# Optimization experiments

Hardware: AMD Instinct MI355X
Metric: run time of the kernel (lower is better)

Reference implementation:

```python
import jax, jax.numpy as jnp
import numpy as np

NUM_EXPERTS = 8
HIDDEN = 2048
INTER = 4096
TOKENS = 4096
TOP_K = 2


def setup_inputs() -> dict:
    key = jax.random.key(0)
    ks = jax.random.split(key, 6)
    x = jax.random.normal(ks[0], (TOKENS, HIDDEN), dtype=jnp.float32)
    expert_weights = jax.random.uniform(ks[1], (TOKENS, TOP_K), dtype=jnp.float32)
    expert_indices = jax.random.randint(ks[2], (TOKENS, TOP_K), 0, NUM_EXPERTS)
    # kaiming_uniform-ish init for stacked expert weights
    b1 = float(np.sqrt(6.0 / HIDDEN))
    b2 = float(np.sqrt(6.0 / INTER))
    w1_stacked = jax.random.uniform(ks[3], (NUM_EXPERTS, HIDDEN, INTER), minval=-b1, maxval=b1, dtype=jnp.float32)
    w2_stacked = jax.random.uniform(ks[4], (NUM_EXPERTS, INTER, HIDDEN), minval=-b2, maxval=b2, dtype=jnp.float32)
    w3_stacked = jax.random.uniform(ks[5], (NUM_EXPERTS, HIDDEN, INTER), minval=-b1, maxval=b1, dtype=jnp.float32)
    return {
        "x": x,
        "expert_weights": expert_weights,
        "w1_stacked": w1_stacked,
        "w2_stacked": w2_stacked,
        "w3_stacked": w3_stacked,
        "expert_indices": expert_indices,
        "num_experts_per_tok": TOP_K,
    }


def reference(x, expert_weights, w1_stacked, w2_stacked, w3_stacked, expert_indices, num_experts_per_tok):
    # out[t] = sum_k expert_weights[t,k] * SwiGLU_FFN_{expert_indices[t,k]}(x[t])
    # Loop over the small fixed expert set; masked weighted combine per expert.
    num_experts = w1_stacked.shape[0]
    out = jnp.zeros_like(x)
    for e in range(num_experts):
        gate = jax.nn.silu(x @ w1_stacked[e])          # [T, I]
        up = x @ w3_stacked[e]                          # [T, I]
        y = (gate * up) @ w2_stacked[e]                 # [T, H]
        # per-token routing weight for expert e (sum over top-k slots)
        w_e = jnp.sum(jnp.where(expert_indices == e, expert_weights, 0.0), axis=1)  # [T]
        out = out + w_e[:, None] * y
    return out
```

## Files before the change

### kernel.cpp

```cpp
#include <hip/hip_runtime.h>
#include <hip/hip_bf16.h>
#include <cstdint>

#define T_TOKENS 4096
#define HID      2048
#define INTER    4096
#define NEXP     8
#define TOPK     2
#define NPAIRS   (T_TOKENS * TOPK)
#define BM 256
#define BN 128
#define BK 64
#define MAXROWS  (NPAIRS + NEXP * BM)
#define NRB2     32

typedef __attribute__((ext_vector_type(8))) short   short8;
typedef __attribute__((ext_vector_type(4))) float   f32x4;
typedef __attribute__((ext_vector_type(8))) ushort  ushort8v;

static __device__ __forceinline__ ushort f2bf(float f) {
    __hip_bfloat16 b = __float2bfloat16(f);
    return __builtin_bit_cast(ushort, b);
}

typedef const __attribute__((address_space(1))) unsigned char ga_u8;
typedef __attribute__((address_space(3))) unsigned char       la_u8;
static __device__ __forceinline__ void gl_lds16(const void* g, void* l) {
    __builtin_amdgcn_global_load_lds((ga_u8*)g, (la_u8*)l, 16, 0, 0);
}

#define SBAR() do { __builtin_amdgcn_sched_barrier(0); \
                    __builtin_amdgcn_s_barrier(); \
                    __builtin_amdgcn_sched_barrier(0); \
                    asm volatile("" ::: "memory"); } while (0)
#define VMCNT(n) do { asm volatile("s_waitcnt vmcnt(" #n ")" ::: "memory"); \
                      __builtin_amdgcn_sched_barrier(0); } while (0)

__global__ void route_kernel(const int* __restrict__ eidx,
                             const float* __restrict__ ew,
                             int* __restrict__ cnt, int* __restrict__ pbase,
                             int* __restrict__ tokl, float* __restrict__ wgtl) {
    __shared__ int s_cnt[NEXP];
    __shared__ int s_pos[NEXP];
    __shared__ int s_base[NEXP];
    int tid = threadIdx.x;
    if (tid < NEXP) { s_cnt[tid] = 0; s_pos[tid] = 0; }
    __syncthreads();
    for (int p = tid; p < NPAIRS; p += blockDim.x)
        atomicAdd(&s_cnt[eidx[p]], 1);
    __syncthreads();
    if (tid == 0) {
        int b = 0;
        for (int e = 0; e < NEXP; ++e) {
            s_base[e] = b;
            cnt[e]    = s_cnt[e];
            pbase[e]  = b;
            b += (s_cnt[e] + BM - 1) / BM * BM;
        }
        pbase[NEXP] = b;
    }
    __syncthreads();
    for (int p = tid; p < NPAIRS; p += blockDim.x) {
        int e   = eidx[p];
        int pos = atomicAdd(&s_pos[e], 1);
        int row = s_base[e] + pos;
        tokl[row] = p >> 1;
        wgtl[row] = ew[p];
    }
}

__global__ __launch_bounds__(256) void cvt_x_kernel(const float* __restrict__ x,
                                                    ushort* __restrict__ xbf) {
    int i = (blockIdx.x * 256 + threadIdx.x) * 8;
    float4 a = *reinterpret_cast<const float4*>(x + i);
    float4 b = *reinterpret_cast<const float4*>(x + i + 4);
    ushort8v o;
    o[0] = f2bf(a.x); o[1] = f2bf(a.y); o[2] = f2bf(a.z); o[3] = f2bf(a.w);
    o[4] = f2bf(b.x); o[5] = f2bf(b.y); o[6] = f2bf(b.z); o[7] = f2bf(b.w);
    *reinterpret_cast<ushort8v*>(xbf + i) = o;
}

__global__ __launch_bounds__(256) void transpose_cvt_kernel(
        const float* __restrict__ src, ushort* __restrict__ dst,
        int K, int N, int c0, int CN, long estride) {
    int ez = blockIdx.z;
    const float* s = src + (size_t)ez * estride;
    ushort* d = dst + (size_t)ez * CN * K;
    int nb = blockIdx.x * 64 + c0;
    int kb = blockIdx.y * 64;
    __shared__ ushort t[64][72];
    int tid = threadIdx.x;
    int kr = tid >> 2;
    int ns = tid & 3;
    #pragma unroll
    for (int p = 0; p < 4; ++p) {
        int f = ns + p * 4;
        float4 v = *reinterpret_cast<const float4*>(&s[(size_t)(kb + kr) * N + nb + f * 4]);
        t[f * 4 + 0][kr] = f2bf(v.x);
        t[f * 4 + 1][kr] = f2bf(v.y);
        t[f * 4 + 2][kr] = f2bf(v.z);
        t[f * 4 + 3][kr] = f2bf(v.w);
    }
    __syncthreads();
    int nr = tid >> 2;
    #pragma unroll
    for (int p = 0; p < 2; ++p) {
        int ks = ((tid & 3) + p * 4) * 8;
        ushort8v v8 = *reinterpret_cast<const ushort8v*>(&t[nr][ks]);
        *reinterpret_cast<ushort8v*>(&d[(size_t)(nb - c0 + nr) * K + kb + ks]) = v8;
    }
}

__global__ __launch_bounds__(512, 2) void ffn1_kernel(
        const ushort* __restrict__ xbf,
        const ushort* __restrict__ wT1, const ushort* __restrict__ wT3,
        const int* __restrict__ cnt, const int* __restrict__ pbase,
        const int* __restrict__ tokl, ushort* __restrict__ h,
        int ncb, int c0) {
    int d = blockIdx.x;
    int xcd = d & 7, q = d >> 3;
    int gq = q / NRB2, rb = q % NRB2;
    int g = gq * 8 + xcd;
    int ez = g / ncb, cb = g - ez * ncb;
    int ce = cnt[ez];
    int e = ez;
    (void)e;
    int r0 = rb * BM;
    if (r0 >= ce) return;
    int base = pbase[ez];

    __shared__ char lds[131072];
    char* Lb = lds;

    int tid  = threadIdx.x;
    int lane = tid & 63, wid = tid >> 6;
    int wr = (wid >> 1) * 64, wc = (wid & 1) * 64;
    int rlow = lane & 15, khi = lane >> 4;

    int rr = tid >> 3;
    int ss = (tid & 7) ^ (rr & 7);
    const ushort* pA[4];
    #pragma unroll
    for (int i = 0; i < 4; ++i) {
        int row = r0 + i * 64 + rr;
        int tok = (row < ce) ? tokl[base + row] : 0;
        pA[i] = xbf + (size_t)tok * HID + ss * 8;
    }
    size_t wrow = (size_t)ez * ((size_t)ncb * 128) + (size_t)cb * 128;
    const ushort* pB1[2];
    const ushort* pB3[2];
    #pragma unroll
    for (int i = 0; i < 2; ++i) {
        pB1[i] = wT1 + (wrow + i * 64 + rr) * HID + ss * 8;
        pB3[i] = wT3 + (wrow + i * 64 + rr) * HID + ss * 8;
    }
    int ldst = wid << 10;

    int aoffs[4][2], boffs[4][2];
    #pragma unroll
    for (int mi = 0; mi < 4; ++mi)
        #pragma unroll
        for (int kh = 0; kh < 2; ++kh) {
            int sw = (((kh << 2) + khi) ^ (lane & 7)) << 4;
            aoffs[mi][kh] = (wr + mi * 16 + rlow) * 128 + sw;
            boffs[mi][kh] = (wc + mi * 16 + rlow) * 128 + sw;
        }

    f32x4 accg[4][4], accu[4][4];
    #pragma unroll
    for (int i = 0; i < 4; ++i)
        #pragma unroll
        for (int j = 0; j < 4; ++j) { accg[i][j] = (f32x4)0.f; accu[i][j] = (f32x4)0.f; }

    {
        char* L = Lb;
        #pragma unroll
        for (int i = 0; i < 4; ++i) gl_lds16(pA[i], L + i * 8192 + ldst);
        #pragma unroll
        for (int i = 0; i < 2; ++i) gl_lds16(pB1[i], L + 32768 + i * 8192 + ldst);
        #pragma unroll
        for (int i = 0; i < 2; ++i) gl_lds16(pB3[i], L + 49152 + i * 8192 + ldst);
    }

    const int NT = HID / BK;
    #pragma unroll 1
    for (int t = 0; t < NT; ++t) {
        char* Lc = Lb + ((t & 1) ? 65536 : 0);
        char* Ln = Lb + ((t & 1) ? 0 : 65536);
        int adv = (t + 1) * 64;
        bool more = (t + 1 < NT);
        if (more) {
            gl_lds16(pA[0] + adv, Ln + 0 * 8192 + ldst);
            gl_lds16(pA[1] + adv, Ln + 1 * 8192 + ldst);
            VMCNT(2);
        } else {
            VMCNT(0);
        }
        SBAR();
        short8 af[4][2];
        #pragma unroll
        for (int mi = 0; mi < 4; ++mi)
            #pragma unroll
            for (int kh = 0; kh < 2; ++kh)
                af[mi][kh] = *reinterpret_cast<const short8*>(Lc + aoffs[mi][kh]);
        short8 bf[2][2];
        #pragma unroll
        for (int ni = 0; ni < 2; ++ni)
            #pragma unroll
            for (int kh = 0; kh < 2; ++kh)
                bf[ni][kh] = *reinterpret_cast<const short8*>(Lc + 32768 + boffs[ni][kh]);
        if (more) {
            gl_lds16(pA[2] + adv, Ln + 2 * 8192 + ldst);
            gl_lds16(pA[3] + adv, Ln + 3 * 8192 + ldst);
        }
        __builtin_amdgcn_s_setprio(1);
        #pragma unroll
        for (int ni = 0; ni < 2; ++ni)
            #pragma unroll
            for (int mi = 0; mi < 4; ++mi)
                #pragma unroll
                for (int kh = 0; kh < 2; ++kh)
                    accg[mi][ni] = __builtin_amdgcn_mfma_f32_16x16x32_bf16(af[mi][kh], bf[ni][kh], accg[mi][ni], 0, 0, 0);
        __builtin_amdgcn_s_setprio(0);
        SBAR();
        #pragma unroll
        for (int ni = 0; ni < 2; ++ni)
            #pragma unroll
            for (int kh = 0; kh < 2; ++kh)
                bf[ni][kh] = *reinterpret_cast<const short8*>(Lc + 49152 + boffs[ni][kh]);
        if (more) {
            gl_lds16(pB1[0] + adv, Ln + 32768 + ldst);
            gl_lds16(pB1[1] + adv, Ln + 32768 + 8192 + ldst);
        }
        __builtin_amdgcn_s_setprio(1);
        #pragma unroll
        for (int ni = 0; ni < 2; ++ni)
            #pragma unroll
            for (int mi = 0; mi < 4; ++mi)
                #pragma unroll
                for (int kh = 0; kh < 2; ++kh)
                    accu[mi][ni] = __builtin_amdgcn_mfma_f32_16x16x32_bf16(af[mi][kh], bf[ni][kh], accu[mi][ni], 0, 0, 0);
        __builtin_amdgcn_s_setprio(0);
        SBAR();
        #pragma unroll
        for (int ni = 0; ni < 2; ++ni)
            #pragma unroll
            for (int kh = 0; kh < 2; ++kh)
                bf[ni][kh] = *reinterpret_cast<const short8*>(Lc + 32768 + boffs[ni + 2][kh]);
        if (more) {
            gl_lds16(pB3[0] + adv, Ln + 49152 + ldst);
            gl_lds16(pB3[1] + adv, Ln + 49152 + 8192 + ldst);
        }
        __builtin_amdgcn_s_setprio(1);
        #pragma unroll
        for (int ni = 0; ni < 2; ++ni)
            #pragma unroll
            for (int mi = 0; mi < 4; ++mi)
                #pragma unroll
                for (int kh = 0; kh < 2; ++kh)
                    accg[mi][ni + 2] = __builtin_amdgcn_mfma_f32_16x16x32_bf16(af[mi][kh], bf[ni][kh], accg[mi][ni + 2], 0, 0, 0);
        __builtin_amdgcn_s_setprio(0);
        SBAR();
        #pragma unroll
        for (int ni = 0; ni < 2; ++ni)
            #pragma unroll
            for (int kh = 0; kh < 2; ++kh)
                bf[ni][kh] = *reinterpret_cast<const short8*>(Lc + 49152 + boffs[ni + 2][kh]);
        __builtin_amdgcn_s_setprio(1);
        #pragma unroll
        for (int ni = 0; ni < 2; ++ni)
            #pragma unroll
            for (int mi = 0; mi < 4; ++mi)
                #pragma unroll
                for (int kh = 0; kh < 2; ++kh)
                    accu[mi][ni + 2] = __builtin_amdgcn_mfma_f32_16x16x32_bf16(af[mi][kh], bf[ni][kh], accu[mi][ni + 2], 0, 0, 0);
        __builtin_amdgcn_s_setprio(0);
        SBAR();
    }

    int hcol = c0 + cb * 128 + wc + rlow;
    #pragma unroll
    for (int mi = 0; mi < 4; ++mi) {
        #pragma unroll
        for (int q2 = 0; q2 < 4; ++q2) {
            int r = r0 + wr + mi * 16 + khi * 4 + q2;
            if (r >= ce) continue;
            ushort* hp = h + (size_t)(base + r) * INTER + hcol;
            #pragma unroll
            for (int ni = 0; ni < 4; ++ni) {
                float gg = accg[mi][ni][q2];
                float uu = accu[mi][ni][q2];
                float s = gg / (1.f + __expf(-gg));
                hp[ni * 16] = f2bf(s * uu);
            }
        }
    }
}

__global__ __launch_bounds__(512, 2) void ffn2_kernel(
        const ushort* __restrict__ h,
        const ushort* __restrict__ wT2,
        const int* __restrict__ cnt, const int* __restrict__ pbase,
        const int* __restrict__ tokl, const float* __restrict__ wgtl,
        float* __restrict__ out, int ncb, int c0) {
    int d = blockIdx.x;
    int xcd = d & 7, q = d >> 3;
    int gq = q / NRB2, rb = q % NRB2;
    int g = gq * 8 + xcd;
    int ez = g / ncb, cb = g - ez * ncb;
    int ce = cnt[ez];
    int r0 = rb * BM;
    if (r0 >= ce) return;
    int base = pbase[ez];

    __shared__ char lds[98304];
    char* Lb = lds;

    int tid  = threadIdx.x;
    int lane = tid & 63, wid = tid >> 6;
    int wr = (wid >> 1) * 64, wc = (wid & 1) * 64;
    int rlow = lane & 15, khi = lane >> 4;

    int rr = tid >> 3;
    int ss = (tid & 7) ^ (rr & 7);
    const ushort* pA[4];
    #pragma unroll
    for (int i = 0; i < 4; ++i)
        pA[i] = h + (size_t)(base + r0 + i * 64 + rr) * INTER + ss * 8;
    size_t wrow = (size_t)ez * ((size_t)ncb * 128) + (size_t)cb * 128;
    const ushort* pB[2];
    #pragma unroll
    for (int i = 0; i < 2; ++i)
        pB[i] = wT2 + (wrow + i * 64 + rr) * INTER + ss * 8;
    int ldst = wid << 10;

    int aoffs[4][2], boffs[4][2];
    #pragma unroll
    for (int mi = 0; mi < 4; ++mi)
        #pragma unroll
        for (int kh = 0; kh < 2; ++kh) {
            int sw = (((kh << 2) + khi) ^ (lane & 7)) << 4;
            aoffs[mi][kh] = (wr + mi * 16 + rlow) * 128 + sw;
            boffs[mi][kh] = (wc + mi * 16 + rlow) * 128 + sw;
        }

    f32x4 acc[4][4];
    #pragma unroll
    for (int i = 0; i < 4; ++i)
        #pragma unroll
        for (int j = 0; j < 4; ++j) acc[i][j] = (f32x4)0.f;

    {
        char* L = Lb;
        #pragma unroll
        for (int i = 0; i < 4; ++i) gl_lds16(pA[i], L + i * 8192 + ldst);
        #pragma unroll
        for (int i = 0; i < 2; ++i) gl_lds16(pB[i], L + 32768 + i * 8192 + ldst);
    }

    const int NT = INTER / BK;
    #pragma unroll 1
    for (int t = 0; t < NT; ++t) {
        char* Lc = Lb + ((t & 1) ? 49152 : 0);
        char* Ln = Lb + ((t & 1) ? 0 : 49152);
        int adv = (t + 1) * 64;
        bool more = (t + 1 < NT);
        if (more) {
            gl_lds16(pA[0] + adv, Ln + 0 * 8192 + ldst);
            gl_lds16(pA[1] + adv, Ln + 1 * 8192 + ldst);
            VMCNT(2);
        } else {
            VMCNT(0);
        }
        SBAR();
        short8 af[4][2];
        #pragma unroll
        for (int mi = 0; mi < 4; ++mi)
            #pragma unroll
            for (int kh = 0; kh < 2; ++kh)
                af[mi][kh] = *reinterpret_cast<const short8*>(Lc + aoffs[mi][kh]);
        short8 bf[2][2];
        #pragma unroll
        for (int ni = 0; ni < 2; ++ni)
            #pragma unroll
            for (int kh = 0; kh < 2; ++kh)
                bf[ni][kh] = *reinterpret_cast<const short8*>(Lc + 32768 + boffs[ni][kh]);
        if (more) {
            gl_lds16(pA[2] + adv, Ln + 2 * 8192 + ldst);
            gl_lds16(pA[3] + adv, Ln + 3 * 8192 + ldst);
        }
        __builtin_amdgcn_s_setprio(1);
        #pragma unroll
        for (int ni = 0; ni < 2; ++ni)
            #pragma unroll
            for (int mi = 0; mi < 4; ++mi)
                #pragma unroll
                for (int kh = 0; kh < 2; ++kh)
                    acc[mi][ni] = __builtin_amdgcn_mfma_f32_16x16x32_bf16(af[mi][kh], bf[ni][kh], acc[mi][ni], 0, 0, 0);
        __builtin_amdgcn_s_setprio(0);
        SBAR();
        #pragma unroll
        for (int ni = 0; ni < 2; ++ni)
            #pragma unroll
            for (int kh = 0; kh < 2; ++kh)
                bf[ni][kh] = *reinterpret_cast<const short8*>(Lc + 32768 + boffs[ni + 2][kh]);
        if (more) {
            gl_lds16(pB[0] + adv, Ln + 32768 + ldst);
            gl_lds16(pB[1] + adv, Ln + 32768 + 8192 + ldst);
        }
        __builtin_amdgcn_s_setprio(1);
        #pragma unroll
        for (int ni = 0; ni < 2; ++ni)
            #pragma unroll
            for (int mi = 0; mi < 4; ++mi)
                #pragma unroll
                for (int kh = 0; kh < 2; ++kh)
                    acc[mi][ni + 2] = __builtin_amdgcn_mfma_f32_16x16x32_bf16(af[mi][kh], bf[ni][kh], acc[mi][ni + 2], 0, 0, 0);
        __builtin_amdgcn_s_setprio(0);
        SBAR();
    }

    int ocol = c0 + cb * 128 + wc + rlow;
    #pragma unroll
    for (int mi = 0; mi < 4; ++mi) {
        #pragma unroll
        for (int q2 = 0; q2 < 4; ++q2) {
            int r = r0 + wr + mi * 16 + khi * 4 + q2;
            if (r >= ce) continue;
            int tok  = tokl[base + r];
            float wv = wgtl[base + r];
            float* op = out + (size_t)tok * HID + ocol;
            #pragma unroll
            for (int ni = 0; ni < 4; ++ni)
                atomicAdd(&op[ni * 16], wv * acc[mi][ni][q2]);
        }
    }
}

extern "C" void kernel_launch(void* const* d_in, const int* in_sizes, int n_in,
                              void* d_out, int out_size, void* d_ws, size_t ws_size,
                              hipStream_t stream) {
    (void)in_sizes; (void)n_in; (void)out_size;
    const float* x   = (const float*)d_in[0];
    const float* ew  = (const float*)d_in[1];
    const float* w1  = (const float*)d_in[2];
    const float* w2  = (const float*)d_in[3];
    const float* w3  = (const float*)d_in[4];
    const int*  eidx = (const int*)d_in[5];
    float* out = (float*)d_out;

    int*   cnt   = (int*)d_ws;
    int*   pbase = cnt + 8;
    int*   tokl  = cnt + 32;
    float* wgtl  = (float*)(tokl + MAXROWS);
    ushort* xbf  = (ushort*)((((uintptr_t)(wgtl + MAXROWS)) + 255) & ~(uintptr_t)255);
    ushort* h    = xbf + (size_t)T_TOKENS * HID;
    ushort* region = h + (size_t)MAXROWS * INTER;
    size_t region_bytes = ws_size - ((char*)region - (char*)d_ws);

    hipMemsetAsync(d_out, 0, (size_t)T_TOKENS * HID * sizeof(float), stream);
    route_kernel<<<1, 256, 0, stream>>>(eidx, ew, cnt, pbase, tokl, wgtl);
    cvt_x_kernel<<<T_TOKENS * HID / 8 / 256, 256, 0, stream>>>(x, xbf);

    const size_t per_e1 = (size_t)2 * INTER * HID * 2;
    const size_t per_e2 = (size_t)HID * INTER * 2;

    if (region_bytes >= per_e1) {
        int EG = (int)(region_bytes / per_e1); if (EG > 8) EG = 8;
        for (int g = 0; g < NEXP; g += EG) {
            int ne = (NEXP - g < EG) ? (NEXP - g) : EG;
            ushort* wt1 = region;
            ushort* wt3 = region + (size_t)ne * INTER * HID;
            transpose_cvt_kernel<<<dim3(INTER / 64, HID / 64, ne), 256, 0, stream>>>(
                w1 + (size_t)g * HID * INTER, wt1, HID, INTER, 0, INTER, (long)HID * INTER);
            transpose_cvt_kernel<<<dim3(INTER / 64, HID / 64, ne), 256, 0, stream>>>(
                w3 + (size_t)g * HID * INTER, wt3, HID, INTER, 0, INTER, (long)HID * INTER);
            ffn1_kernel<<<NRB2 * ne * (INTER / BN), 512, 0, stream>>>(
                xbf, wt1, wt3, cnt + g, pbase + g, tokl, h, INTER / BN, 0);
        }
    } else {
        const int CN = 1024;
        for (int e = 0; e < NEXP; ++e) {
            for (int c = 0; c < INTER; c += CN) {
                ushort* wt1 = region;
                ushort* wt3 = region + (size_t)CN * HID;
                transpose_cvt_kernel<<<dim3(CN / 64, HID / 64, 1), 256, 0, stream>>>(
                    w1 + (size_t)e * HID * INTER, wt1, HID, INTER, c, CN, (long)HID * INTER);
                transpose_cvt_kernel<<<dim3(CN / 64, HID / 64, 1), 256, 0, stream>>>(
                    w3 + (size_t)e * HID * INTER, wt3, HID, INTER, c, CN, (long)HID * INTER);
                ffn1_kernel<<<NRB2 * (CN / BN), 512, 0, stream>>>(
                    xbf, wt1, wt3, cnt + e, pbase + e, tokl, h, CN / BN, c);
            }
        }
    }

    if (region_bytes >= per_e2) {
        int EG = (int)(region_bytes / per_e2); if (EG > 8) EG = 8;
        for (int g = 0; g < NEXP; g += EG) {
            int ne = (NEXP - g < EG) ? (NEXP - g) : EG;
            ushort* wt2 = region;
            transpose_cvt_kernel<<<dim3(HID / 64, INTER / 64, ne), 256, 0, stream>>>(
                w2 + (size_t)g * INTER * HID, wt2, INTER, HID, 0, HID, (long)INTER * HID);
            ffn2_kernel<<<NRB2 * ne * (HID / BN), 512, 0, stream>>>(
                h, wt2, cnt + g, pbase + g, tokl, wgtl, out, HID / BN, 0);
        }
    } else {
        const int CN = 1024;
        for (int e = 0; e < NEXP; ++e) {
            for (int c = 0; c < HID; c += CN) {
                ushort* wt2 = region;
                transpose_cvt_kernel<<<dim3(CN / 64, INTER / 64, 1), 256, 0, stream>>>(
                    w2 + (size_t)e * INTER * HID, wt2, INTER, HID, c, CN, (long)INTER * HID);
                ffn2_kernel<<<NRB2 * (CN / BN), 512, 0, stream>>>(
                    h, wt2, cnt + e, pbase + e, tokl, wgtl, out, CN / BN, c);
            }
        }
    }
}
```

Baseline: 873.0 us.

## Unify FFN GEMMs into templated 256x256 tile kernel with split gate/up passes

Replaces the fused gate+up kernel and the separate down-projection kernel with one templated GEMM using 256x256 tiles, 8 waves arranged 2x4, and a reworked four-phase pipeline in which A and B loads are staggered two tiles ahead. The gate and up projections become two separate launches: the first writes the gate result to h in bf16, the second reads it back and applies SiLU times up. The larger tile is meant to raise MFMA work per LDS byte. In exchange x is loaded twice, h makes an extra bf16 round trip through memory, and the gate value is rounded to bf16 before SiLU.

```diff
diff --git a/kernel.cpp b/kernel.cpp
--- a/kernel.cpp
+++ b/kernel.cpp
@@ -8,10 +8,8 @@
 #define NEXP     8
 #define TOPK     2
 #define NPAIRS   (T_TOKENS * TOPK)
-#define BM 256
-#define BN 128
-#define BK 64
-#define MAXROWS  (NPAIRS + NEXP * BM)
+#define BMR      256
+#define MAXROWS  (NPAIRS + NEXP * BMR)
 #define NRB2     32
 
 typedef __attribute__((ext_vector_type(8))) short   short8;
@@ -21,6 +19,9 @@
 static __device__ __forceinline__ ushort f2bf(float f) {
     __hip_bfloat16 b = __float2bfloat16(f);
     return __builtin_bit_cast(ushort, b);
+}
+static __device__ __forceinline__ float bf2f(ushort u) {
+    return __builtin_bit_cast(float, ((uint)u) << 16);
 }
 
 typedef const __attribute__((address_space(1))) unsigned char ga_u8;
@@ -35,6 +36,8 @@
                     asm volatile("" ::: "memory"); } while (0)
 #define VMCNT(n) do { asm volatile("s_waitcnt vmcnt(" #n ")" ::: "memory"); \
                       __builtin_amdgcn_sched_barrier(0); } while (0)
+#define LGKM0() do { asm volatile("s_waitcnt lgkmcnt(0)" ::: "memory"); \
+                     __builtin_amdgcn_sched_barrier(0); } while (0)
 
 __global__ void route_kernel(const int* __restrict__ eidx,
                              const float* __restrict__ ew,
@@ -55,7 +58,7 @@
             s_base[e] = b;
             cnt[e]    = s_cnt[e];
             pbase[e]  = b;
-            b += (s_cnt[e] + BM - 1) / BM * BM;
+            b += (s_cnt[e] + BMR - 1) / BMR * BMR;
         }
         pbase[NEXP] = b;
     }
@@ -111,328 +114,187 @@
     }
 }
 
-__global__ __launch_bounds__(512, 2) void ffn1_kernel(
-        const ushort* __restrict__ xbf,
-        const ushort* __restrict__ wT1, const ushort* __restrict__ wT3,
+template<int MODE>
+__global__ __launch_bounds__(512, 2) void gemm_kernel(
+        const ushort* __restrict__ Asrc, const ushort* __restrict__ wT,
         const int* __restrict__ cnt, const int* __restrict__ pbase,
-        const int* __restrict__ tokl, ushort* __restrict__ h,
-        int ncb, int c0) {
+        const int* __restrict__ tokl, const float* __restrict__ wgtl,
+        ushort* __restrict__ hbuf, float* __restrict__ out,
+        int ncb, int c0, int ng) {
+    constexpr int K  = (MODE == 2) ? INTER : HID;
+    constexpr int NT = K / 64;
+
     int d = blockIdx.x;
     int xcd = d & 7, q = d >> 3;
     int gq = q / NRB2, rb = q % NRB2;
     int g = gq * 8 + xcd;
+    if (g >= ng) return;
     int ez = g / ncb, cb = g - ez * ncb;
     int ce = cnt[ez];
-    int e = ez;
-    (void)e;
-    int r0 = rb * BM;
+    int r0 = rb * BMR;
     if (r0 >= ce) return;
     int base = pbase[ez];
 
     __shared__ char lds[131072];
-    char* Lb = lds;
 
     int tid  = threadIdx.x;
     int lane = tid & 63, wid = tid >> 6;
-    int wr = (wid >> 1) * 64, wc = (wid & 1) * 64;
+    int wm = wid >> 2, wn = wid & 3;
+    int wr = wm * 128, wc = wn * 64;
     int rlow = lane & 15, khi = lane >> 4;
 
     int rr = tid >> 3;
-    int ss = (tid & 7) ^ (rr & 7);
+    int ssl = (tid & 7) ^ (rr & 7);
     const ushort* pA[4];
     #pragma unroll
     for (int i = 0; i < 4; ++i) {
-        int row = r0 + i * 64 + rr;
-        int tok = (row < ce) ? tokl[base + row] : 0;
-        pA[i] = xbf + (size_t)tok * HID + ss * 8;
-    }
-    size_t wrow = (size_t)ez * ((size_t)ncb * 128) + (size_t)cb * 128;
-    const ushort* pB1[2];
-    const ushort* pB3[2];
-    #pragma unroll
-    for (int i = 0; i < 2; ++i) {
-        pB1[i] = wT1 + (wrow + i * 64 + rr) * HID + ss * 8;
-        pB3[i] = wT3 + (wrow + i * 64 + rr) * HID + ss * 8;
-    }
-    int ldst = wid << 10;
-
-    int aoffs[4][2], boffs[4][2];
-    #pragma unroll
-    for (int mi = 0; mi < 4; ++mi)
-        #pragma unroll
-        for (int kh = 0; kh < 2; ++kh) {
-            int sw = (((kh << 2) + khi) ^ (lane & 7)) << 4;
-            aoffs[mi][kh] = (wr + mi * 16 + rlow) * 128 + sw;
-            boffs[mi][kh] = (wc + mi * 16 + rlow) * 128 + sw;
-        }
-
-    f32x4 accg[4][4], accu[4][4];
+        if constexpr (MODE == 2) {
+            pA[i] = Asrc + (size_t)(base + r0 + i * 64 + rr) * K + ssl * 8;
+        } else {
+            int row = r0 + i * 64 + rr;
+            int tok = (row < ce) ? tokl[base + row] : 0;
+            pA[i] = Asrc + (size_t)tok * K + ssl * 8;
+        }
+    }
+    size_t wcol = (size_t)ez * ((size_t)ncb * 256) + (size_t)cb * 256;
+    const ushort* pB[4];
     #pragma unroll
     for (int i = 0; i < 4; ++i)
-        #pragma unroll
-        for (int j = 0; j < 4; ++j) { accg[i][j] = (f32x4)0.f; accu[i][j] = (f32x4)0.f; }
-
-    {
-        char* L = Lb;
-        #pragma unroll
-        for (int i = 0; i < 4; ++i) gl_lds16(pA[i], L + i * 8192 + ldst);
-        #pragma unroll
-        for (int i = 0; i < 2; ++i) gl_lds16(pB1[i], L + 32768 + i * 8192 + ldst);
-        #pragma unroll
-        for (int i = 0; i < 2; ++i) gl_lds16(pB3[i], L + 49152 + i * 8192 + ldst);
-    }
-
-    const int NT = HID / BK;
+        pB[i] = wT + (wcol + i * 64 + rr) * K + ssl * 8;
+
+    int abase = wm * 16384;
+    int bbase = 32768 + (wn >> 1) * 16384;
+    int aoff[8], boff[4];
+    #pragma unroll
+    for (int mi = 0; mi < 8; ++mi) {
+        int arow = mi * 16 + rlow;
+        aoff[mi] = abase + arow * 128 + ((khi ^ (arow & 7)) << 4);
+    }
+    #pragma unroll
+    for (int ni = 0; ni < 4; ++ni) {
+        int brow = (wn & 1) * 64 + ni * 16 + rlow;
+        boff[ni] = bbase + brow * 128 + ((khi ^ (brow & 7)) << 4);
+    }
+
+    f32x4 acc[8][4];
+    #pragma unroll
+    for (int i = 0; i < 8; ++i)
+        #pragma unroll
+        for (int j = 0; j < 4; ++j) acc[i][j] = (f32x4)0.f;
+
+    auto stA = [&](int db, int h, int t) {
+        char* d0 = lds + db * 65536 + h * 16384 + tid * 16;
+        gl_lds16(pA[h * 2 + 0] + t * 64, d0);
+        gl_lds16(pA[h * 2 + 1] + t * 64, d0 + 8192);
+    };
+    auto stB = [&](int db, int h, int t) {
+        char* d0 = lds + db * 65536 + 32768 + h * 16384 + tid * 16;
+        gl_lds16(pB[h * 2 + 0] + t * 64, d0);
+        gl_lds16(pB[h * 2 + 1] + t * 64, d0 + 8192);
+    };
+
+    stA(0, 0, 0); stA(0, 1, 0); stB(0, 0, 0); stB(0, 1, 0);
+    stA(1, 0, 1); stA(1, 1, 1);
+    VMCNT(4);
+    SBAR();
+
     #pragma unroll 1
     for (int t = 0; t < NT; ++t) {
-        char* Lc = Lb + ((t & 1) ? 65536 : 0);
-        char* Ln = Lb + ((t & 1) ? 0 : 65536);
-        int adv = (t + 1) * 64;
-        bool more = (t + 1 < NT);
-        if (more) {
-            gl_lds16(pA[0] + adv, Ln + 0 * 8192 + ldst);
-            gl_lds16(pA[1] + adv, Ln + 1 * 8192 + ldst);
-            VMCNT(2);
-        } else {
-            VMCNT(0);
-        }
-        SBAR();
-        short8 af[4][2];
-        #pragma unroll
-        for (int mi = 0; mi < 4; ++mi)
-            #pragma unroll
-            for (int kh = 0; kh < 2; ++kh)
-                af[mi][kh] = *reinterpret_cast<const short8*>(Lc + aoffs[mi][kh]);
-        short8 bf[2][2];
+        int db = t & 1, nb = db ^ 1;
+        const char* L = lds + db * 65536;
+        int t1 = (t + 1 < NT) ? t + 1 : NT - 1;
+        int t2 = (t + 2 < NT) ? t + 2 : NT - 1;
+        short8 af0[8], af1[8], bfr[2];
+
+        #pragma unroll
+        for (int mi = 0; mi < 8; ++mi)
+            af0[mi] = *reinterpret_cast<const short8*>(L + aoff[mi]);
+        bfr[0] = *reinterpret_cast<const short8*>(L + boff[0]);
+        bfr[1] = *reinterpret_cast<const short8*>(L + boff[1]);
+        stB(nb, 0, t1);
+        SBAR(); LGKM0();
+        __builtin_amdgcn_s_setprio(1);
         #pragma unroll
         for (int ni = 0; ni < 2; ++ni)
             #pragma unroll
-            for (int kh = 0; kh < 2; ++kh)
-                bf[ni][kh] = *reinterpret_cast<const short8*>(Lc + 32768 + boffs[ni][kh]);
-        if (more) {
-            gl_lds16(pA[2] + adv, Ln + 2 * 8192 + ldst);
-            gl_lds16(pA[3] + adv, Ln + 3 * 8192 + ldst);
-        }
+            for (int mi = 0; mi < 8; ++mi)
+                acc[mi][ni] = __builtin_amdgcn_mfma_f32_16x16x32_bf16(af0[mi], bfr[ni], acc[mi][ni], 0, 0, 0);
+        __builtin_amdgcn_s_setprio(0);
+        SBAR();
+
+        #pragma unroll
+        for (int mi = 0; mi < 8; ++mi)
+            af1[mi] = *reinterpret_cast<const short8*>(L + (aoff[mi] ^ 64));
+        bfr[0] = *reinterpret_cast<const short8*>(L + (boff[0] ^ 64));
+        bfr[1] = *reinterpret_cast<const short8*>(L + (boff[1] ^ 64));
+        stB(nb, 1, t1);
+        SBAR(); LGKM0();
         __builtin_amdgcn_s_setprio(1);
         #pragma unroll
         for (int ni = 0; ni < 2; ++ni)
             #pragma unroll
-            for (int mi = 0; mi < 4; ++mi)
-                #pragma unroll
-                for (int kh = 0; kh < 2; ++kh)
-                    accg[mi][ni] = __builtin_amdgcn_mfma_f32_16x16x32_bf16(af[mi][kh], bf[ni][kh], accg[mi][ni], 0, 0, 0);
+            for (int mi = 0; mi < 8; ++mi)
+                acc[mi][ni] = __builtin_amdgcn_mfma_f32_16x16x32_bf16(af1[mi], bfr[ni], acc[mi][ni], 0, 0, 0);
         __builtin_amdgcn_s_setprio(0);
         SBAR();
+
+        bfr[0] = *reinterpret_cast<const short8*>(L + boff[2]);
+        bfr[1] = *reinterpret_cast<const short8*>(L + boff[3]);
+        stA(db, 0, t2);
+        SBAR(); LGKM0();
+        __builtin_amdgcn_s_setprio(1);
         #pragma unroll
         for (int ni = 0; ni < 2; ++ni)
             #pragma unroll
-            for (int kh = 0; kh < 2; ++kh)
-                bf[ni][kh] = *reinterpret_cast<const short8*>(Lc + 49152 + boffs[ni][kh]);
-        if (more) {
-            gl_lds16(pB1[0] + adv, Ln + 32768 + ldst);
-            gl_lds16(pB1[1] + adv, Ln + 32768 + 8192 + ldst);
-        }
+            for (int mi = 0; mi < 8; ++mi)
+                acc[mi][ni + 2] = __builtin_amdgcn_mfma_f32_16x16x32_bf16(af0[mi], bfr[ni], acc[mi][ni + 2], 0, 0, 0);
+        __builtin_amdgcn_s_setprio(0);
+        SBAR();
+
+        bfr[0] = *reinterpret_cast<const short8*>(L + (boff[2] ^ 64));
+        bfr[1] = *reinterpret_cast<const short8*>(L + (boff[3] ^ 64));
+        stA(db, 1, t2);
+        SBAR(); LGKM0();
         __builtin_amdgcn_s_setprio(1);
         #pragma unroll
         for (int ni = 0; ni < 2; ++ni)
             #pragma unroll
-            for (int mi = 0; mi < 4; ++mi)
-                #pragma unroll
-                for (int kh = 0; kh < 2; ++kh)
-                    accu[mi][ni] = __builtin_amdgcn_mfma_f32_16x16x32_bf16(af[mi][kh], bf[ni][kh], accu[mi][ni], 0, 0, 0);
+            for (int mi = 0; mi < 8; ++mi)
+                acc[mi][ni + 2] = __builtin_amdgcn_mfma_f32_16x16x32_bf16(af1[mi], bfr[ni], acc[mi][ni + 2], 0, 0, 0);
         __builtin_amdgcn_s_setprio(0);
+        VMCNT(4);
         SBAR();
-        #pragma unroll
-        for (int ni = 0; ni < 2; ++ni)
-            #pragma unroll
-            for (int kh = 0; kh < 2; ++kh)
-                bf[ni][kh] = *reinterpret_cast<const short8*>(Lc + 32768 + boffs[ni + 2][kh]);
-        if (more) {
-            gl_lds16(pB3[0] + adv, Ln + 49152 + ldst);
-            gl_lds16(pB3[1] + adv, Ln + 49152 + 8192 + ldst);
-        }
-        __builtin_amdgcn_s_setprio(1);
-        #pragma unroll
-        for (int ni = 0; ni < 2; ++ni)
-            #pragma unroll
-            for (int mi = 0; mi < 4; ++mi)
-                #pragma unroll
-                for (int kh = 0; kh < 2; ++kh)
-                    accg[mi][ni + 2] = __builtin_amdgcn_mfma_f32_16x16x32_bf16(af[mi][kh], bf[ni][kh], accg[mi][ni + 2], 0, 0, 0);
-        __builtin_amdgcn_s_setprio(0);
-        SBAR();
-        #pragma unroll
-        for (int ni = 0; ni < 2; ++ni)
-            #pragma unroll
-            for (int kh = 0; kh < 2; ++kh)
-                bf[ni][kh] = *reinterpret_cast<const short8*>(Lc + 49152 + boffs[ni + 2][kh]);
-        __builtin_amdgcn_s_setprio(1);
-        #pragma unroll
-        for (int ni = 0; ni < 2; ++ni)
-            #pragma unroll
-            for (int mi = 0; mi < 4; ++mi)
-                #pragma unroll
-                for (int kh = 0; kh < 2; ++kh)
-                    accu[mi][ni + 2] = __builtin_amdgcn_mfma_f32_16x16x32_bf16(af[mi][kh], bf[ni][kh], accu[mi][ni + 2], 0, 0, 0);
-        __builtin_amdgcn_s_setprio(0);
-        SBAR();
-    }
-
-    int hcol = c0 + cb * 128 + wc + rlow;
-    #pragma unroll
-    for (int mi = 0; mi < 4; ++mi) {
+    }
+    VMCNT(0);
+
+    int colb = c0 + cb * 256 + wc + rlow;
+    #pragma unroll
+    for (int mi = 0; mi < 8; ++mi) {
         #pragma unroll
         for (int q2 = 0; q2 < 4; ++q2) {
             int r = r0 + wr + mi * 16 + khi * 4 + q2;
             if (r >= ce) continue;
-            ushort* hp = h + (size_t)(base + r) * INTER + hcol;
-            #pragma unroll
-            for (int ni = 0; ni < 4; ++ni) {
-                float gg = accg[mi][ni][q2];
-                float uu = accu[mi][ni][q2];
-                float s = gg / (1.f + __expf(-gg));
-                hp[ni * 16] = f2bf(s * uu);
+            if constexpr (MODE == 0) {
+                ushort* hp = hbuf + (size_t)(base + r) * INTER + colb;
+                #pragma unroll
+                for (int ni = 0; ni < 4; ++ni)
+                    hp[ni * 16] = f2bf(acc[mi][ni][q2]);
+            } else if constexpr (MODE == 1) {
+                ushort* hp = hbuf + (size_t)(base + r) * INTER + colb;
+                #pragma unroll
+                for (int ni = 0; ni < 4; ++ni) {
+                    float gg = bf2f(hp[ni * 16]);
+                    float s  = gg / (1.f + __expf(-gg));
+                    hp[ni * 16] = f2bf(s * acc[mi][ni][q2]);
+                }
+            } else {
+                int tok  = tokl[base + r];
+                float wv = wgtl[base + r];
+                float* op = out + (size_t)tok * HID + colb;
+                #pragma unroll
+                for (int ni = 0; ni < 4; ++ni)
+                    atomicAdd(&op[ni * 16], wv * acc[mi][ni][q2]);
             }
-        }
-    }
-}
-
-__global__ __launch_bounds__(512, 2) void ffn2_kernel(
-        const ushort* __restrict__ h,
-        const ushort* __restrict__ wT2,
-        const int* __restrict__ cnt, const int* __restrict__ pbase,
-        const int* __restrict__ tokl, const float* __restrict__ wgtl,
-        float* __restrict__ out, int ncb, int c0) {
-    int d = blockIdx.x;
-    int xcd = d & 7, q = d >> 3;
-    int gq = q / NRB2, rb = q % NRB2;
-    int g = gq * 8 + xcd;
-    int ez = g / ncb, cb = g - ez * ncb;
-    int ce = cnt[ez];
-    int r0 = rb * BM;
-    if (r0 >= ce) return;
-    int base = pbase[ez];
-
-    __shared__ char lds[98304];
-    char* Lb = lds;
-
-    int tid  = threadIdx.x;
-    int lane = tid & 63, wid = tid >> 6;
-    int wr = (wid >> 1) * 64, wc = (wid & 1) * 64;
-    int rlow = lane & 15, khi = lane >> 4;
-
-    int rr = tid >> 3;
-    int ss = (tid & 7) ^ (rr & 7);
-    const ushort* pA[4];
-    #pragma unroll
-    for (int i = 0; i < 4; ++i)
-        pA[i] = h + (size_t)(base + r0 + i * 64 + rr) * INTER + ss * 8;
-    size_t wrow = (size_t)ez * ((size_t)ncb * 128) + (size_t)cb * 128;
-    const ushort* pB[2];
-    #pragma unroll
-    for (int i = 0; i < 2; ++i)
-        pB[i] = wT2 + (wrow + i * 64 + rr) * INTER + ss * 8;
-    int ldst = wid << 10;
-
-    int aoffs[4][2], boffs[4][2];
-    #pragma unroll
-    for (int mi = 0; mi < 4; ++mi)
-        #pragma unroll
-        for (int kh = 0; kh < 2; ++kh) {
-            int sw = (((kh << 2) + khi) ^ (lane & 7)) << 4;
-            aoffs[mi][kh] = (wr + mi * 16 + rlow) * 128 + sw;
-            boffs[mi][kh] = (wc + mi * 16 + rlow) * 128 + sw;
-        }
-
-    f32x4 acc[4][4];
-    #pragma unroll
-    for (int i = 0; i < 4; ++i)
-        #pragma unroll
-        for (int j = 0; j < 4; ++j) acc[i][j] = (f32x4)0.f;
-
-    {
-        char* L = Lb;
-        #pragma unroll
-        for (int i = 0; i < 4; ++i) gl_lds16(pA[i], L + i * 8192 + ldst);
-        #pragma unroll
-        for (int i = 0; i < 2; ++i) gl_lds16(pB[i], L + 32768 + i * 8192 + ldst);
-    }
-
-    const int NT = INTER / BK;
-    #pragma unroll 1
-    for (int t = 0; t < NT; ++t) {
-        char* Lc = Lb + ((t & 1) ? 49152 : 0);
-        char* Ln = Lb + ((t & 1) ? 0 : 49152);
-        int adv = (t + 1) * 64;
-        bool more = (t + 1 < NT);
-        if (more) {
-            gl_lds16(pA[0] + adv, Ln + 0 * 8192 + ldst);
-            gl_lds16(pA[1] + adv, Ln + 1 * 8192 + ldst);
-            VMCNT(2);
-        } else {
-            VMCNT(0);
-        }
-        SBAR();
-        short8 af[4][2];
-        #pragma unroll
-        for (int mi = 0; mi < 4; ++mi)
-            #pragma unroll
-            for (int kh = 0; kh < 2; ++kh)
-                af[mi][kh] = *reinterpret_cast<const short8*>(Lc + aoffs[mi][kh]);
-        short8 bf[2][2];
-        #pragma unroll
-        for (int ni = 0; ni < 2; ++ni)
-            #pragma unroll
-            for (int kh = 0; kh < 2; ++kh)
-                bf[ni][kh] = *reinterpret_cast<const short8*>(Lc + 32768 + boffs[ni][kh]);
-        if (more) {
-            gl_lds16(pA[2] + adv, Ln + 2 * 8192 + ldst);
-            gl_lds16(pA[3] + adv, Ln + 3 * 8192 + ldst);
-        }
-        __builtin_amdgcn_s_setprio(1);
-        #pragma unroll
-        for (int ni = 0; ni < 2; ++ni)
-            #pragma unroll
-            for (int mi = 0; mi < 4; ++mi)
-                #pragma unroll
-                for (int kh = 0; kh < 2; ++kh)
-                    acc[mi][ni] = __builtin_amdgcn_mfma_f32_16x16x32_bf16(af[mi][kh], bf[ni][kh], acc[mi][ni], 0, 0, 0);
-        __builtin_amdgcn_s_setprio(0);
-        SBAR();
-        #pragma unroll
-        for (int ni = 0; ni < 2; ++ni)
-            #pragma unroll
-            for (int kh = 0; kh < 2; ++kh)
-                bf[ni][kh] = *reinterpret_cast<const short8*>(Lc + 32768 + boffs[ni + 2][kh]);
-        if (more) {
-            gl_lds16(pB[0] + adv, Ln + 32768 + ldst);
-            gl_lds16(pB[1] + adv, Ln + 32768 + 8192 + ldst);
-        }
-        __builtin_amdgcn_s_setprio(1);
-        #pragma unroll
-        for (int ni = 0; ni < 2; ++ni)
-            #pragma unroll
-            for (int mi = 0; mi < 4; ++mi)
-                #pragma unroll
-                for (int kh = 0; kh < 2; ++kh)
-                    acc[mi][ni + 2] = __builtin_amdgcn_mfma_f32_16x16x32_bf16(af[mi][kh], bf[ni][kh], acc[mi][ni + 2], 0, 0, 0);
-        __builtin_amdgcn_s_setprio(0);
-        SBAR();
-    }
-
-    int ocol = c0 + cb * 128 + wc + rlow;
-    #pragma unroll
-    for (int mi = 0; mi < 4; ++mi) {
-        #pragma unroll
-        for (int q2 = 0; q2 < 4; ++q2) {
-            int r = r0 + wr + mi * 16 + khi * 4 + q2;
-            if (r >= ce) continue;
-            int tok  = tokl[base + r];
-            float wv = wgtl[base + r];
-            float* op = out + (size_t)tok * HID + ocol;
-            #pragma unroll
-            for (int ni = 0; ni < 4; ++ni)
-                atomicAdd(&op[ni * 16], wv * acc[mi][ni][q2]);
         }
     }
 }
@@ -475,11 +337,14 @@
                 w1 + (size_t)g * HID * INTER, wt1, HID, INTER, 0, INTER, (long)HID * INTER);
             transpose_cvt_kernel<<<dim3(INTER / 64, HID / 64, ne), 256, 0, stream>>>(
                 w3 + (size_t)g * HID * INTER, wt3, HID, INTER, 0, INTER, (long)HID * INTER);
-            ffn1_kernel<<<NRB2 * ne * (INTER / BN), 512, 0, stream>>>(
-                xbf, wt1, wt3, cnt + g, pbase + g, tokl, h, INTER / BN, 0);
+            int ng = ne * (INTER / 256);
+            gemm_kernel<0><<<NRB2 * ng, 512, 0, stream>>>(
+                xbf, wt1, cnt + g, pbase + g, tokl, wgtl, h, out, INTER / 256, 0, ng);
+            gemm_kernel<1><<<NRB2 * ng, 512, 0, stream>>>(
+                xbf, wt3, cnt + g, pbase + g, tokl, wgtl, h, out, INTER / 256, 0, ng);
         }
     } else {
-        const int CN = 1024;
+        const int CN = 2048;
         for (int e = 0; e < NEXP; ++e) {
             for (int c = 0; c < INTER; c += CN) {
                 ushort* wt1 = region;
@@ -488,8 +353,11 @@
                     w1 + (size_t)e * HID * INTER, wt1, HID, INTER, c, CN, (long)HID * INTER);
                 transpose_cvt_kernel<<<dim3(CN / 64, HID / 64, 1), 256, 0, stream>>>(
                     w3 + (size_t)e * HID * INTER, wt3, HID, INTER, c, CN, (long)HID * INTER);
-                ffn1_kernel<<<NRB2 * (CN / BN), 512, 0, stream>>>(
-                    xbf, wt1, wt3, cnt + e, pbase + e, tokl, h, CN / BN, c);
+                int ng = CN / 256;
+                gemm_kernel<0><<<NRB2 * ng, 512, 0, stream>>>(
+                    xbf, wt1, cnt + e, pbase + e, tokl, wgtl, h, out, CN / 256, c, ng);
+                gemm_kernel<1><<<NRB2 * ng, 512, 0, stream>>>(
+                    xbf, wt3, cnt + e, pbase + e, tokl, wgtl, h, out, CN / 256, c, ng);
             }
         }
     }
@@ -501,8 +369,9 @@
             ushort* wt2 = region;
             transpose_cvt_kernel<<<dim3(HID / 64, INTER / 64, ne), 256, 0, stream>>>(
                 w2 + (size_t)g * INTER * HID, wt2, INTER, HID, 0, HID, (long)INTER * HID);
-            ffn2_kernel<<<NRB2 * ne * (HID / BN), 512, 0, stream>>>(
-                h, wt2, cnt + g, pbase + g, tokl, wgtl, out, HID / BN, 0);
+            int ng = ne * (HID / 256);
+            gemm_kernel<2><<<NRB2 * ng, 512, 0, stream>>>(
+                h, wt2, cnt + g, pbase + g, tokl, wgtl, h, out, HID / 256, 0, ng);
         }
     } else {
         const int CN = 1024;
@@ -511,8 +380,10 @@
                 ushort* wt2 = region;
                 transpose_cvt_kernel<<<dim3(CN / 64, INTER / 64, 1), 256, 0, stream>>>(
                     w2 + (size_t)e * INTER * HID, wt2, INTER, HID, c, CN, (long)INTER * HID);
-                ffn2_kernel<<<NRB2 * (CN / BN), 512, 0, stream>>>(
-                    h, wt2, cnt + e, pbase + e, tokl, wgtl, out, CN / BN, c);
+                int ng = CN / 256;
+                int ngp = (ng + 7) / 8 * 8;
+                gemm_kernel<2><<<NRB2 * ngp, 512, 0, stream>>>(
+                    h, wt2, cnt + e, pbase + e, tokl, wgtl, h, out, CN / 256, c, ng);
             }
         }
     }
```

Measured after the change: 877.1 us. About the same (+0.5%).
